# Kernel optimization log

Hardware: AMD Instinct MI355X
Metric: run time of the kernel (lower is better)

## Reference

```python
import jax, jax.numpy as jnp
import numpy as np

B, C, H, W = 8, 256, 64, 64
NUM_LABELS = 16  # labels in {-1, 0..15}; -1 means 'no group'


def setup_inputs() -> dict:
    key = jax.random.key(0)
    kx, kl, kw, kb = jax.random.split(key, 4)
    x = jax.random.normal(kx, (B, C, H, W), dtype=jnp.float32)
    # labels in [-1, NUM_LABELS)
    labels = jax.random.randint(kl, (B * C,), 0, NUM_LABELS + 1) - 1
    # groups=C, kernel 1x1: conv weight is (3C,1,1,1) -> per-output-channel scale; bias (3C,)
    w = jax.random.normal(kw, (3 * C,), dtype=jnp.float32) * 0.5
    b = jax.random.normal(kb, (3 * C,), dtype=jnp.float32) * 0.02
    return {"x": x, "labels": labels, "w": w, "b": b}


def reference(x, labels, w, b):
    # x: (B,C,h,w); labels: (B*C,); w,b: (3C,)
    Bv, Cv, hv, wv = x.shape
    hw = hv * wv
    xf = x.reshape(Bv, Cv, hw)
    # grouped 1x1 conv: out channel o (of 3C) reads input channel o//3
    x_rep = jnp.repeat(xf, 3, axis=1)                      # (B,3C,hw)
    qkv = x_rep * w[None, :, None] + b[None, :, None]      # (B,3C,hw)
    flat = qkv.reshape(Bv * 3 * Cv, hw)                    # matches torch reshape(1,3BC,hw)
    BC = Bv * Cv
    q, k, v = flat[:BC], flat[BC:2 * BC], flat[2 * BC:]    # each (BC, hw)
    valid = labels != -1                                   # (BC,)
    same = (labels[:, None] == labels[None, :]) & valid[:, None] & valid[None, :]
    # per-label-group attention == masked dense attention (softmax over same-label cols only)
    scores = q @ k.T                                       # (BC, BC), no sqrt(d) scaling (as in source)
    neg = jnp.finfo(scores.dtype).min
    scores = jnp.where(same, scores, neg)
    weights = jax.nn.softmax(scores, axis=-1)
    out = weights @ v                                      # (BC, hw)
    out = jnp.where(valid[:, None], out, jnp.zeros((), out.dtype))  # -1 rows stay zero
    return out[None]                                       # (1, BC, hw)
```

## Files before the change

### kernel.cpp

```cpp
#include <hip/hip_runtime.h>
#include <cfloat>

#define B_   8
#define C_   256
#define HW_  4096
#define BC_  2048
#define TC_  768
#define NG_  16
#define MAXG 320
#define UK0  682
#define NUQ  683
#define NUK  684
#define NXU  1366
#define NXALL 2048

#define SPLITK 8
#define NT     11
#define NTILES (NT * NT)
#define KSL    (HW_ / SPLITK)
#define WKC    (KSL / 4)
#define NP1    (NUQ * NUK)

#define MCAP  192
#define CST   192
#define BKP   216

typedef __attribute__((ext_vector_type(8))) short short8;
typedef __attribute__((ext_vector_type(4))) float floatx4;

__device__ __forceinline__ unsigned short f32_to_bf16_rne(float f) {
  unsigned u = __float_as_uint(f);
  unsigned r = (u + 0x7FFFu + ((u >> 16) & 1u)) >> 16;
  return (unsigned short)r;
}

__global__ __launch_bounds__(256) void prep_kernel(
    const float* __restrict__ x, const int* __restrict__ labels,
    unsigned short* __restrict__ xhi, unsigned short* __restrict__ xlo,
    float* __restrict__ sums, int* __restrict__ grp_n,
    int* __restrict__ members, int* __restrict__ posArr, int nhi)
{
  const int t = threadIdx.x;
  if (blockIdx.x < NG_) {
    __shared__ int lab[BC_];
    __shared__ int cnts[256];
    const int g = blockIdx.x;
    for (int idx = t; idx < BC_; idx += 256) lab[idx] = labels[idx];
    __syncthreads();
    const int base = t * 8;
    int cnt = 0;
#pragma unroll
    for (int k = 0; k < 8; k++) cnt += (lab[base + k] == g) ? 1 : 0;
    cnts[t] = cnt;
    for (int off = 1; off < 256; off <<= 1) {
      __syncthreads();
      const int v = (t >= off) ? cnts[t - off] : 0;
      __syncthreads();
      cnts[t] += v;
    }
    __syncthreads();
    int pos = cnts[t] - cnt;
    if (t == 255) grp_n[g] = cnts[255] < MAXG ? cnts[255] : MAXG;
#pragma unroll
    for (int k = 0; k < 8; k++) {
      const int i = base + k;
      if (lab[i] == g) {
        if (pos < MAXG) { members[g * MAXG + pos] = i; posArr[i] = pos; }
        pos++;
      }
    }
    return;
  }

  const int u = blockIdx.x - NG_;
  const float* row = x + (size_t)u * HW_;
  unsigned short* hrow = xhi + (size_t)u * HW_;
  if (u < NXU) {
    unsigned short* lrow = xlo + (size_t)u * HW_;
    float s = 0.f;
#pragma unroll
    for (int i = 0; i < 4; i++) {
      const int col = i * 1024 + t * 4;
      const float4 v = *(const float4*)(row + col);
      s += v.x + v.y + v.z + v.w;
      ushort4 h, l;
      h.x = f32_to_bf16_rne(v.x);
      h.y = f32_to_bf16_rne(v.y);
      h.z = f32_to_bf16_rne(v.z);
      h.w = f32_to_bf16_rne(v.w);
      l.x = f32_to_bf16_rne(v.x - __uint_as_float((unsigned)h.x << 16));
      l.y = f32_to_bf16_rne(v.y - __uint_as_float((unsigned)h.y << 16));
      l.z = f32_to_bf16_rne(v.z - __uint_as_float((unsigned)h.z << 16));
      l.w = f32_to_bf16_rne(v.w - __uint_as_float((unsigned)h.w << 16));
      *(ushort4*)(hrow + col) = h;
      *(ushort4*)(lrow + col) = l;
    }
#pragma unroll
    for (int o = 32; o > 0; o >>= 1) s += __shfl_down(s, o);
    __shared__ float red[4];
    if ((t & 63) == 0) red[t >> 6] = s;
    __syncthreads();
    if (t == 0) sums[u] = red[0] + red[1] + red[2] + red[3];
  } else {
#pragma unroll
    for (int i = 0; i < 4; i++) {
      const int col = i * 1024 + t * 4;
      const float4 v = *(const float4*)(row + col);
      ushort4 h;
      h.x = f32_to_bf16_rne(v.x);
      h.y = f32_to_bf16_rne(v.y);
      h.z = f32_to_bf16_rne(v.z);
      h.w = f32_to_bf16_rne(v.w);
      *(ushort4*)(hrow + col) = h;
    }
  }
}

__global__ __launch_bounds__(256) void gram_mfma_kernel(
    const unsigned short* __restrict__ xhi, const unsigned short* __restrict__ xlo,
    float* __restrict__ P,
    const float* __restrict__ w, const float* __restrict__ bbias,
    const float* __restrict__ sums, const int* __restrict__ grp_n,
    const int* __restrict__ members, float4* __restrict__ gtA,
    float2* __restrict__ gtB)
{
  const int bid  = blockIdx.x;
  const int z    = bid & 7;
  const int tile = bid >> 3;
  const int m0 = (tile % NT) * 64;
  const int n0 = (tile / NT) * 64;

  const int t = threadIdx.x;
  const int wave = t >> 6;
  const int lane = t & 63;
  const int fr = lane & 15;
  const int fq = lane >> 4;

  if (z == 0 && tile < NG_) {
    const int g = tile;
    const int n = grp_n[g];
    for (int p = t; p < n; p += 256) {
      const int j = members[g * MAXG + p];
      const int rk = j + BC_;
      const int jk = rk % TC_;
      const int uk = (rk / TC_) * C_ + jk / 3;
      const int jv = (j + 2 * BC_) % TC_;
      gtA[g * MAXG + p] = make_float4(w[jk], bbias[jk], sums[uk], w[jv]);
      gtB[g * MAXG + p] = make_float2(bbias[jv], __int_as_float(uk - UK0));
    }
  }

  const int kbase = z * KSL + wave * WKC + fq * 8;
  const unsigned short *pah[4], *pal[4], *pbh[4], *pbl[4];
#pragma unroll
  for (int i = 0; i < 4; i++) {
    const int ar = min(m0 + fr + i * 16, NUQ - 1);
    const int br = min(UK0 + n0 + fr + i * 16, NXU - 1);
    pah[i] = xhi + (size_t)ar * HW_ + kbase;
    pal[i] = xlo + (size_t)ar * HW_ + kbase;
    pbh[i] = xhi + (size_t)br * HW_ + kbase;
    pbl[i] = xlo + (size_t)br * HW_ + kbase;
  }

  floatx4 acc[4][4];
#pragma unroll
  for (int i = 0; i < 4; i++)
#pragma unroll
    for (int j = 0; j < 4; j++) acc[i][j] = (floatx4)(0.f);

  for (int kk = 0; kk < WKC; kk += 32) {
    short8 ah[4], al[4], bh[4], bl[4];
#pragma unroll
    for (int i = 0; i < 4; i++) {
      ah[i] = *(const short8*)(pah[i] + kk);
      al[i] = *(const short8*)(pal[i] + kk);
      bh[i] = *(const short8*)(pbh[i] + kk);
      bl[i] = *(const short8*)(pbl[i] + kk);
    }
#pragma unroll
    for (int mt = 0; mt < 4; mt++)
#pragma unroll
      for (int nt = 0; nt < 4; nt++) {
        acc[mt][nt] = __builtin_amdgcn_mfma_f32_16x16x32_bf16(ah[mt], bh[nt], acc[mt][nt], 0, 0, 0);
        acc[mt][nt] = __builtin_amdgcn_mfma_f32_16x16x32_bf16(al[mt], bh[nt], acc[mt][nt], 0, 0, 0);
        acc[mt][nt] = __builtin_amdgcn_mfma_f32_16x16x32_bf16(ah[mt], bl[nt], acc[mt][nt], 0, 0, 0);
      }
  }

  __shared__ float R[2][64][68];
  float* R0 = &R[0][0][0];
  float* R1 = &R[1][0][0];
  if (wave == 0 || wave == 2) {
    float* Rw = (wave == 0) ? R0 : R1;
#pragma unroll
    for (int mt = 0; mt < 4; mt++)
#pragma unroll
      for (int nt = 0; nt < 4; nt++)
#pragma unroll
        for (int r = 0; r < 4; r++)
          Rw[(mt * 16 + fq * 4 + r) * 68 + nt * 16 + fr] = acc[mt][nt][r];
  }
  __syncthreads();
  if (wave == 1 || wave == 3) {
    float* Rw = (wave == 1) ? R0 : R1;
#pragma unroll
    for (int mt = 0; mt < 4; mt++)
#pragma unroll
      for (int nt = 0; nt < 4; nt++)
#pragma unroll
        for (int r = 0; r < 4; r++)
          Rw[(mt * 16 + fq * 4 + r) * 68 + nt * 16 + fr] += acc[mt][nt][r];
  }
  __syncthreads();
  const int em = t >> 2;
  const int en = (t & 3) * 16;
  const int gm = m0 + em;
  if (gm < NUQ) {
    float* dst = P + (size_t)z * NP1 + (size_t)gm * NUK + n0;
#pragma unroll
    for (int i4 = 0; i4 < 4; i4++) {
      const int n = en + i4 * 4;
      if (n0 + n < NUK) {
        float4 v;
        v.x = R0[em * 68 + n + 0] + R1[em * 68 + n + 0];
        v.y = R0[em * 68 + n + 1] + R1[em * 68 + n + 1];
        v.z = R0[em * 68 + n + 2] + R1[em * 68 + n + 2];
        v.w = R0[em * 68 + n + 3] + R1[em * 68 + n + 3];
        *(float4*)(dst + n) = v;
      }
    }
  }
}

__global__ __launch_bounds__(256) void gram_reduce_kernel(
    const float* __restrict__ P, float* __restrict__ S)
{
  const int idx = (blockIdx.x * 256 + threadIdx.x) * 4;
  if (idx < NP1) {
    float4 s = *(const float4*)(P + idx);
#pragma unroll
    for (int sl = 1; sl < SPLITK; sl++) {
      const float4 a = *(const float4*)(P + (size_t)sl * NP1 + idx);
      s.x += a.x; s.y += a.y; s.z += a.z; s.w += a.w;
    }
    *(float4*)(S + idx) = s;
  }
}

__device__ __forceinline__ float blockReduceMax(float v, float* red) {
#pragma unroll
  for (int o = 32; o > 0; o >>= 1) v = fmaxf(v, __shfl_down(v, o));
  if ((threadIdx.x & 63) == 0) red[threadIdx.x >> 6] = v;
  __syncthreads();
  v = fmaxf(fmaxf(red[0], red[1]), fmaxf(red[2], red[3]));
  __syncthreads();
  return v;
}
__device__ __forceinline__ float blockReduceSum(float v, float* red) {
#pragma unroll
  for (int o = 32; o > 0; o >>= 1) v += __shfl_down(v, o);
  if ((threadIdx.x & 63) == 0) red[threadIdx.x >> 6] = v;
  __syncthreads();
  v = red[0] + red[1] + red[2] + red[3];
  __syncthreads();
  return v;
}

__global__ __launch_bounds__(256) void softmax_kernel(
    const int* __restrict__ labels, const float* __restrict__ w,
    const float* __restrict__ bbias, const float* __restrict__ sums,
    const float* __restrict__ S, const int* __restrict__ grp_n,
    const int* __restrict__ posArr, const float4* __restrict__ gtA,
    const float2* __restrict__ gtB, unsigned short* __restrict__ coefh,
    float* __restrict__ cb, float* __restrict__ out)
{
  const int i = blockIdx.x;
  const int t = threadIdx.x;
  const int g = labels[i];
  if (g < 0) {
    const float4 z = make_float4(0.f, 0.f, 0.f, 0.f);
    float4* orow = (float4*)(out + (size_t)i * HW_);
    for (int cidx = t; cidx < HW_ / 4; cidx += 256) orow[cidx] = z;
    return;
  }
  __shared__ float red[4];
  const int n   = grp_n[g];
  const int jq  = i % TC_;
  const int uqi = (i / TC_) * C_ + jq / 3;
  const float wq = w[jq], bq = bbias[jq];
  const float sq = sums[uqi];
  const float* Srow = S + (size_t)uqi * NUK;

  const int jj0 = t, jj1 = t + 256;
  float4 A0, A1; float2 B0, B1;
  float s0 = -FLT_MAX, s1 = -FLT_MAX;
  if (jj0 < n) {
    A0 = gtA[g * MAXG + jj0];
    B0 = gtB[g * MAXG + jj0];
    s0 = wq * A0.x * Srow[__float_as_int(B0.y)] + (wq * A0.y) * sq +
         (bq * A0.x) * A0.z + (bq * A0.y) * 4096.f;
  }
  if (jj1 < n) {
    A1 = gtA[g * MAXG + jj1];
    B1 = gtB[g * MAXG + jj1];
    s1 = wq * A1.x * Srow[__float_as_int(B1.y)] + (wq * A1.y) * sq +
         (bq * A1.x) * A1.z + (bq * A1.y) * 4096.f;
  }
  const float mx = blockReduceMax(fmaxf(s0, s1), red);
  const float e0 = (jj0 < n) ? expf(s0 - mx) : 0.f;
  const float e1 = (jj1 < n) ? expf(s1 - mx) : 0.f;
  const float tot = blockReduceSum(e0 + e1, red);
  const float inv = 1.f / tot;

  const int pos = posArr[i];
  unsigned short* crow = coefh + ((size_t)g * MCAP + pos) * CST;
  float lcb = 0.f;
  if (jj0 < n) {
    const float wgt = e0 * inv;
    if (pos < MCAP && jj0 < CST) crow[jj0] = f32_to_bf16_rne(wgt * A0.w);
    lcb += wgt * B0.x;
  } else if (pos < MCAP && jj0 < CST) {
    crow[jj0] = 0;
  }
  if (jj1 < n) {
    const float wgt = e1 * inv;
    lcb += wgt * B1.x;
  }
  const float cbi = blockReduceSum(lcb, red);
  if (t == 0) cb[i] = cbi;
}

__global__ __launch_bounds__(256) void out_mfma_kernel(
    const float* __restrict__ x, const unsigned short* __restrict__ xh,
    const unsigned short* __restrict__ coefh,
    const float* __restrict__ cb, const int* __restrict__ grp_n,
    const int* __restrict__ members, float* __restrict__ out)
{
  const int g  = blockIdx.x;
  const int c0 = blockIdx.y * 64;
  const int n  = min(grp_n[g], MCAP);
  if (n == 0) return;
  const int Kceil = (n + 31) & ~31;
  const int nk8 = Kceil >> 3;
  const int t = threadIdx.x;
  const int wave = t >> 6;
  const int lane = t & 63;
  const int fr = lane & 15;
  const int fq = lane >> 4;

  __shared__ unsigned short Bt[64][BKP];
  __shared__ int   mem[MCAP];
  __shared__ float cbs[MCAP];

  if (t < n) {
    const int j = members[g * MAXG + t];
    mem[t] = j;
    cbs[t] = cb[j];
  }
  __syncthreads();

  {
    const int colq = t & 15;
    const int kcb  = t >> 4;
    for (int kc = kcb; kc < nk8; kc += 16) {
      if (xh) {
        ushort4 hv[8];
#pragma unroll
        for (int j = 0; j < 8; j++) {
          const int k = kc * 8 + j;
          if (k < n) {
            const int jm = mem[k];
            const int rv = jm + 2 * BC_;
            const int uv = (rv / TC_) * C_ + (rv % TC_) / 3;
            hv[j] = *(const ushort4*)(xh + (size_t)uv * HW_ + c0 + colq * 4);
          } else {
            hv[j] = make_ushort4(0, 0, 0, 0);
          }
        }
#pragma unroll
        for (int c = 0; c < 4; c++) {
          short8 pk;
          pk[0] = (short)(c == 0 ? hv[0].x : c == 1 ? hv[0].y : c == 2 ? hv[0].z : hv[0].w);
          pk[1] = (short)(c == 0 ? hv[1].x : c == 1 ? hv[1].y : c == 2 ? hv[1].z : hv[1].w);
          pk[2] = (short)(c == 0 ? hv[2].x : c == 1 ? hv[2].y : c == 2 ? hv[2].z : hv[2].w);
          pk[3] = (short)(c == 0 ? hv[3].x : c == 1 ? hv[3].y : c == 2 ? hv[3].z : hv[3].w);
          pk[4] = (short)(c == 0 ? hv[4].x : c == 1 ? hv[4].y : c == 2 ? hv[4].z : hv[4].w);
          pk[5] = (short)(c == 0 ? hv[5].x : c == 1 ? hv[5].y : c == 2 ? hv[5].z : hv[5].w);
          pk[6] = (short)(c == 0 ? hv[6].x : c == 1 ? hv[6].y : c == 2 ? hv[6].z : hv[6].w);
          pk[7] = (short)(c == 0 ? hv[7].x : c == 1 ? hv[7].y : c == 2 ? hv[7].z : hv[7].w);
          *(short8*)&Bt[colq * 4 + c][kc * 8] = pk;
        }
      } else {
        float4 vals[8];
#pragma unroll
        for (int j = 0; j < 8; j++) {
          const int k = kc * 8 + j;
          if (k < n) {
            const int jm = mem[k];
            const int rv = jm + 2 * BC_;
            const int uv = (rv / TC_) * C_ + (rv % TC_) / 3;
            vals[j] = *(const float4*)(x + (size_t)uv * HW_ + c0 + colq * 4);
          } else {
            vals[j] = make_float4(0.f, 0.f, 0.f, 0.f);
          }
        }
#pragma unroll
        for (int c = 0; c < 4; c++) {
          short8 pk;
          pk[0] = (short)f32_to_bf16_rne(c == 0 ? vals[0].x : c == 1 ? vals[0].y : c == 2 ? vals[0].z : vals[0].w);
          pk[1] = (short)f32_to_bf16_rne(c == 0 ? vals[1].x : c == 1 ? vals[1].y : c == 2 ? vals[1].z : vals[1].w);
          pk[2] = (short)f32_to_bf16_rne(c == 0 ? vals[2].x : c == 1 ? vals[2].y : c == 2 ? vals[2].z : vals[2].w);
          pk[3] = (short)f32_to_bf16_rne(c == 0 ? vals[3].x : c == 1 ? vals[3].y : c == 2 ? vals[3].z : vals[3].w);
          pk[4] = (short)f32_to_bf16_rne(c == 0 ? vals[4].x : c == 1 ? vals[4].y : c == 2 ? vals[4].z : vals[4].w);
          pk[5] = (short)f32_to_bf16_rne(c == 0 ? vals[5].x : c == 1 ? vals[5].y : c == 2 ? vals[5].z : vals[5].w);
          pk[6] = (short)f32_to_bf16_rne(c == 0 ? vals[6].x : c == 1 ? vals[6].y : c == 2 ? vals[6].z : vals[6].w);
          pk[7] = (short)f32_to_bf16_rne(c == 0 ? vals[7].x : c == 1 ? vals[7].y : c == 2 ? vals[7].z : vals[7].w);
          *(short8*)&Bt[colq * 4 + c][kc * 8] = pk;
        }
      }
    }
  }
  __syncthreads();

  const int colw = wave * 16 + fr;

  for (int m0 = 0; m0 < n; m0 += 32) {
    floatx4 acc0 = (floatx4)(0.f), acc1 = (floatx4)(0.f);
    const unsigned short* pa0 = coefh + ((size_t)g * MCAP + m0 + fr) * CST + fq * 8;
    const unsigned short* pa1 = pa0 + 16 * CST;
    for (int k = 0; k < Kceil; k += 32) {
      const short8 a0 = *(const short8*)(pa0 + k);
      const short8 a1 = *(const short8*)(pa1 + k);
      const short8 b  = *(const short8*)&Bt[colw][fq * 8 + k];
      acc0 = __builtin_amdgcn_mfma_f32_16x16x32_bf16(a0, b, acc0, 0, 0, 0);
      acc1 = __builtin_amdgcn_mfma_f32_16x16x32_bf16(a1, b, acc1, 0, 0, 0);
    }
#pragma unroll
    for (int r = 0; r < 4; r++) {
      int m = m0 + fq * 4 + r;
      if (m < n) out[(size_t)mem[m] * HW_ + c0 + colw] = acc0[r] + cbs[m];
      m += 16;
      if (m < n) out[(size_t)mem[m] * HW_ + c0 + colw] = acc1[r] + cbs[m];
    }
  }
}

extern "C" void kernel_launch(void* const* d_in, const int* in_sizes, int n_in,
                              void* d_out, int out_size, void* d_ws, size_t ws_size,
                              hipStream_t stream)
{
  const float* x      = (const float*)d_in[0];
  const int*   labels = (const int*)d_in[1];
  const float* w      = (const float*)d_in[2];
  const float* bb     = (const float*)d_in[3];
  float* out = (float*)d_out;

  char* wsb = (char*)d_ws;
  size_t off = 0;
  auto carve = [&](size_t bytes) -> void* {
    off = (off + 255) & ~(size_t)255;
    void* p = wsb + off;
    off += bytes;
    return p;
  };
  float* sums    = (float*)carve(NXU * sizeof(float));
  float* S       = (float*)carve((size_t)NP1 * sizeof(float));
  float* P       = (float*)carve((size_t)SPLITK * NP1 * sizeof(float));
  int*   grp_n   = (int*)carve(NG_ * sizeof(int));
  int*   members = (int*)carve((size_t)NG_ * MAXG * sizeof(int));
  int*   posArr  = (int*)carve(BC_ * sizeof(int));
  unsigned short* coefh = (unsigned short*)carve((size_t)NG_ * MCAP * CST * sizeof(unsigned short));
  float* cb      = (float*)carve(BC_ * sizeof(float));
  float4* gtA    = (float4*)carve((size_t)NG_ * MAXG * sizeof(float4));
  float2* gtB    = (float2*)carve((size_t)NG_ * MAXG * sizeof(float2));

  const int big = ws_size >= (size_t)47 * 1024 * 1024;
  const int nhi = big ? NXALL : NXU;
  unsigned short* xhi = (unsigned short*)carve((size_t)nhi * HW_ * sizeof(unsigned short));
  unsigned short* xlo = (unsigned short*)carve((size_t)NXU * HW_ * sizeof(unsigned short));

  prep_kernel<<<NG_ + nhi, 256, 0, stream>>>(x, labels, xhi, xlo, sums,
                                             grp_n, members, posArr, nhi);
  gram_mfma_kernel<<<NTILES * SPLITK, 256, 0, stream>>>(
      xhi, xlo, P, w, bb, sums, grp_n, members, gtA, gtB);
  gram_reduce_kernel<<<(NP1 / 4 + 255) / 256, 256, 0, stream>>>(P, S);
  softmax_kernel<<<BC_, 256, 0, stream>>>(labels, w, bb, sums, S, grp_n,
                                          posArr, gtA, gtB, coefh, cb, out);
  out_mfma_kernel<<<dim3(NG_, HW_ / 64), 256, 0, stream>>>(
      x, big ? xhi : (const unsigned short*)nullptr, coefh, cb, grp_n,
      members, out);
}
```

Before: 161.8 us.

## Replace split-bf16 Gram MFMA with per-row int8 hi/lo quantized i8 MFMA

Each input row is quantized to a 16-bit integer using a per-row max-abs scale, then split into high and low int8 bytes. The Gram product becomes three i32 16x16x64 int8 MFMAs in place of three bf16 16x16x32 MFMAs, which halves operand bytes and doubles K per instruction. The per-row scales are applied in the split-K reduce. The prep kernel now stages rows in shared memory and writes bf16 only for rows the output kernel needs, which changes precision behaviour and adds shared-memory pressure in prep.

```diff
diff --git a/kernel.cpp b/kernel.cpp
--- a/kernel.cpp
+++ b/kernel.cpp
@@ -13,6 +13,7 @@
 #define NUK  684
 #define NXU  1366
 #define NXALL 2048
+#define VLO  1280
 
 #define SPLITK 8
 #define NT     11
@@ -20,6 +21,7 @@
 #define KSL    (HW_ / SPLITK)
 #define WKC    (KSL / 4)
 #define NP1    (NUQ * NUK)
+#define QMAX   32639
 
 #define MCAP  192
 #define CST   192
@@ -27,6 +29,7 @@
 
 typedef __attribute__((ext_vector_type(8))) short short8;
 typedef __attribute__((ext_vector_type(4))) float floatx4;
+typedef __attribute__((ext_vector_type(4))) int   intx4;
 
 __device__ __forceinline__ unsigned short f32_to_bf16_rne(float f) {
   unsigned u = __float_as_uint(f);
@@ -36,9 +39,11 @@
 
 __global__ __launch_bounds__(256) void prep_kernel(
     const float* __restrict__ x, const int* __restrict__ labels,
-    unsigned short* __restrict__ xhi, unsigned short* __restrict__ xlo,
-    float* __restrict__ sums, int* __restrict__ grp_n,
-    int* __restrict__ members, int* __restrict__ posArr, int nhi)
+    char* __restrict__ q8h, char* __restrict__ q8l,
+    unsigned short* __restrict__ xhi, float* __restrict__ sums,
+    float* __restrict__ scA, float* __restrict__ scB,
+    int* __restrict__ grp_n, int* __restrict__ members,
+    int* __restrict__ posArr, int nhi)
 {
   const int t = threadIdx.x;
   if (blockIdx.x < NG_) {
@@ -73,35 +78,73 @@
   }
 
   const int u = blockIdx.x - NG_;
+  if (u >= nhi) return;
   const float* row = x + (size_t)u * HW_;
-  unsigned short* hrow = xhi + (size_t)u * HW_;
+
   if (u < NXU) {
-    unsigned short* lrow = xlo + (size_t)u * HW_;
-    float s = 0.f;
+    __shared__ float xs[HW_];
+    __shared__ float red[4];
+    float s = 0.f, mx = 0.f;
 #pragma unroll
     for (int i = 0; i < 4; i++) {
       const int col = i * 1024 + t * 4;
       const float4 v = *(const float4*)(row + col);
+      *(float4*)(xs + col) = v;
       s += v.x + v.y + v.z + v.w;
-      ushort4 h, l;
-      h.x = f32_to_bf16_rne(v.x);
-      h.y = f32_to_bf16_rne(v.y);
-      h.z = f32_to_bf16_rne(v.z);
-      h.w = f32_to_bf16_rne(v.w);
-      l.x = f32_to_bf16_rne(v.x - __uint_as_float((unsigned)h.x << 16));
-      l.y = f32_to_bf16_rne(v.y - __uint_as_float((unsigned)h.y << 16));
-      l.z = f32_to_bf16_rne(v.z - __uint_as_float((unsigned)h.z << 16));
-      l.w = f32_to_bf16_rne(v.w - __uint_as_float((unsigned)h.w << 16));
-      *(ushort4*)(hrow + col) = h;
-      *(ushort4*)(lrow + col) = l;
+      mx = fmaxf(mx, fmaxf(fmaxf(fabsf(v.x), fabsf(v.y)),
+                           fmaxf(fabsf(v.z), fabsf(v.w))));
     }
 #pragma unroll
     for (int o = 32; o > 0; o >>= 1) s += __shfl_down(s, o);
-    __shared__ float red[4];
     if ((t & 63) == 0) red[t >> 6] = s;
     __syncthreads();
-    if (t == 0) sums[u] = red[0] + red[1] + red[2] + red[3];
+    const float rowsum = red[0] + red[1] + red[2] + red[3];
+    __syncthreads();
+#pragma unroll
+    for (int o = 32; o > 0; o >>= 1) mx = fmaxf(mx, __shfl_down(mx, o));
+    if ((t & 63) == 0) red[t >> 6] = mx;
+    __syncthreads();
+    const float bmax = fmaxf(fmaxf(fmaxf(red[0], red[1]),
+                                   fmaxf(red[2], red[3])), 1e-20f);
+    if (t == 0) {
+      sums[u] = rowsum;
+      const float sc = bmax / (float)QMAX;
+      if (u < NUQ)  scA[u] = sc;
+      if (u >= UK0) scB[u - UK0] = sc;
+    }
+    const float sinv = (float)QMAX / bmax;
+    char* hrow = q8h + (size_t)u * HW_;
+    char* lrow = q8l + (size_t)u * HW_;
+#pragma unroll
+    for (int i = 0; i < 4; i++) {
+      const int col = i * 1024 + t * 4;
+      char4 hc, lc;
+#pragma unroll
+      for (int j = 0; j < 4; j++) {
+        int q = __float2int_rn(xs[col + j] * sinv);
+        q = q > QMAX ? QMAX : (q < -QMAX ? -QMAX : q);
+        const int h = (q + 128) >> 8;
+        ((char*)&hc)[j] = (char)h;
+        ((char*)&lc)[j] = (char)(q - (h << 8));
+      }
+      *(char4*)(hrow + col) = hc;
+      *(char4*)(lrow + col) = lc;
+    }
+    if (xhi && u >= VLO) {
+      unsigned short* hb = xhi + (size_t)u * HW_;
+#pragma unroll
+      for (int i = 0; i < 4; i++) {
+        const int col = i * 1024 + t * 4;
+        ushort4 h;
+        h.x = f32_to_bf16_rne(xs[col + 0]);
+        h.y = f32_to_bf16_rne(xs[col + 1]);
+        h.z = f32_to_bf16_rne(xs[col + 2]);
+        h.w = f32_to_bf16_rne(xs[col + 3]);
+        *(ushort4*)(hb + col) = h;
+      }
+    }
   } else {
+    unsigned short* hb = xhi + (size_t)u * HW_;
 #pragma unroll
     for (int i = 0; i < 4; i++) {
       const int col = i * 1024 + t * 4;
@@ -111,13 +154,13 @@
       h.y = f32_to_bf16_rne(v.y);
       h.z = f32_to_bf16_rne(v.z);
       h.w = f32_to_bf16_rne(v.w);
-      *(ushort4*)(hrow + col) = h;
+      *(ushort4*)(hb + col) = h;
     }
   }
 }
 
 __global__ __launch_bounds__(256) void gram_mfma_kernel(
-    const unsigned short* __restrict__ xhi, const unsigned short* __restrict__ xlo,
+    const char* __restrict__ q8h, const char* __restrict__ q8l,
     float* __restrict__ P,
     const float* __restrict__ w, const float* __restrict__ bbias,
     const float* __restrict__ sums, const int* __restrict__ grp_n,
@@ -150,40 +193,40 @@
     }
   }
 
-  const int kbase = z * KSL + wave * WKC + fq * 8;
-  const unsigned short *pah[4], *pal[4], *pbh[4], *pbl[4];
+  const int kbase = z * KSL + wave * WKC + fq * 16;
+  const char *pah[4], *pal[4], *pbh[4], *pbl[4];
 #pragma unroll
   for (int i = 0; i < 4; i++) {
     const int ar = min(m0 + fr + i * 16, NUQ - 1);
     const int br = min(UK0 + n0 + fr + i * 16, NXU - 1);
-    pah[i] = xhi + (size_t)ar * HW_ + kbase;
-    pal[i] = xlo + (size_t)ar * HW_ + kbase;
-    pbh[i] = xhi + (size_t)br * HW_ + kbase;
-    pbl[i] = xlo + (size_t)br * HW_ + kbase;
-  }
-
-  floatx4 acc[4][4];
+    pah[i] = q8h + (size_t)ar * HW_ + kbase;
+    pal[i] = q8l + (size_t)ar * HW_ + kbase;
+    pbh[i] = q8h + (size_t)br * HW_ + kbase;
+    pbl[i] = q8l + (size_t)br * HW_ + kbase;
+  }
+
+  intx4 acch[4][4], accx[4][4];
 #pragma unroll
   for (int i = 0; i < 4; i++)
 #pragma unroll
-    for (int j = 0; j < 4; j++) acc[i][j] = (floatx4)(0.f);
-
-  for (int kk = 0; kk < WKC; kk += 32) {
-    short8 ah[4], al[4], bh[4], bl[4];
+    for (int j = 0; j < 4; j++) { acch[i][j] = (intx4)(0); accx[i][j] = (intx4)(0); }
+
+  for (int kk = 0; kk < WKC; kk += 64) {
+    intx4 ah[4], al[4], bh[4], bl[4];
 #pragma unroll
     for (int i = 0; i < 4; i++) {
-      ah[i] = *(const short8*)(pah[i] + kk);
-      al[i] = *(const short8*)(pal[i] + kk);
-      bh[i] = *(const short8*)(pbh[i] + kk);
-      bl[i] = *(const short8*)(pbl[i] + kk);
+      ah[i] = *(const intx4*)(pah[i] + kk);
+      al[i] = *(const intx4*)(pal[i] + kk);
+      bh[i] = *(const intx4*)(pbh[i] + kk);
+      bl[i] = *(const intx4*)(pbl[i] + kk);
     }
 #pragma unroll
     for (int mt = 0; mt < 4; mt++)
 #pragma unroll
       for (int nt = 0; nt < 4; nt++) {
-        acc[mt][nt] = __builtin_amdgcn_mfma_f32_16x16x32_bf16(ah[mt], bh[nt], acc[mt][nt], 0, 0, 0);
-        acc[mt][nt] = __builtin_amdgcn_mfma_f32_16x16x32_bf16(al[mt], bh[nt], acc[mt][nt], 0, 0, 0);
-        acc[mt][nt] = __builtin_amdgcn_mfma_f32_16x16x32_bf16(ah[mt], bl[nt], acc[mt][nt], 0, 0, 0);
+        acch[mt][nt] = __builtin_amdgcn_mfma_i32_16x16x64_i8(ah[mt], bh[nt], acch[mt][nt], 0, 0, 0);
+        accx[mt][nt] = __builtin_amdgcn_mfma_i32_16x16x64_i8(ah[mt], bl[nt], accx[mt][nt], 0, 0, 0);
+        accx[mt][nt] = __builtin_amdgcn_mfma_i32_16x16x64_i8(al[mt], bh[nt], accx[mt][nt], 0, 0, 0);
       }
   }
 
@@ -198,7 +241,8 @@
       for (int nt = 0; nt < 4; nt++)
 #pragma unroll
         for (int r = 0; r < 4; r++)
-          Rw[(mt * 16 + fq * 4 + r) * 68 + nt * 16 + fr] = acc[mt][nt][r];
+          Rw[(mt * 16 + fq * 4 + r) * 68 + nt * 16 + fr] =
+              65536.f * (float)acch[mt][nt][r] + 256.f * (float)accx[mt][nt][r];
   }
   __syncthreads();
   if (wave == 1 || wave == 3) {
@@ -209,7 +253,8 @@
       for (int nt = 0; nt < 4; nt++)
 #pragma unroll
         for (int r = 0; r < 4; r++)
-          Rw[(mt * 16 + fq * 4 + r) * 68 + nt * 16 + fr] += acc[mt][nt][r];
+          Rw[(mt * 16 + fq * 4 + r) * 68 + nt * 16 + fr] +=
+              65536.f * (float)acch[mt][nt][r] + 256.f * (float)accx[mt][nt][r];
   }
   __syncthreads();
   const int em = t >> 2;
@@ -233,7 +278,8 @@
 }
 
 __global__ __launch_bounds__(256) void gram_reduce_kernel(
-    const float* __restrict__ P, float* __restrict__ S)
+    const float* __restrict__ P, float* __restrict__ S,
+    const float* __restrict__ scA, const float* __restrict__ scB)
 {
   const int idx = (blockIdx.x * 256 + threadIdx.x) * 4;
   if (idx < NP1) {
@@ -243,6 +289,11 @@
       const float4 a = *(const float4*)(P + (size_t)sl * NP1 + idx);
       s.x += a.x; s.y += a.y; s.z += a.z; s.w += a.w;
     }
+    const int m = idx / NUK;
+    const int n = idx - m * NUK;
+    const float sa = scA[m];
+    const float4 sb = *(const float4*)(scB + n);
+    s.x *= sa * sb.x; s.y *= sa * sb.y; s.z *= sa * sb.z; s.w *= sa * sb.w;
     *(float4*)(S + idx) = s;
   }
 }
@@ -464,6 +515,8 @@
     return p;
   };
   float* sums    = (float*)carve(NXU * sizeof(float));
+  float* scA     = (float*)carve(NUQ * sizeof(float));
+  float* scB     = (float*)carve(NUK * sizeof(float));
   float* S       = (float*)carve((size_t)NP1 * sizeof(float));
   float* P       = (float*)carve((size_t)SPLITK * NP1 * sizeof(float));
   int*   grp_n   = (int*)carve(NG_ * sizeof(int));
@@ -473,20 +526,22 @@
   float* cb      = (float*)carve(BC_ * sizeof(float));
   float4* gtA    = (float4*)carve((size_t)NG_ * MAXG * sizeof(float4));
   float2* gtB    = (float2*)carve((size_t)NG_ * MAXG * sizeof(float2));
+  char*  q8h     = (char*)carve((size_t)NXU * HW_);
+  char*  q8l     = (char*)carve((size_t)NXU * HW_);
 
   const int big = ws_size >= (size_t)47 * 1024 * 1024;
+  unsigned short* xhi = big
+      ? (unsigned short*)carve((size_t)NXALL * HW_ * sizeof(unsigned short))
+      : (unsigned short*)nullptr;
   const int nhi = big ? NXALL : NXU;
-  unsigned short* xhi = (unsigned short*)carve((size_t)nhi * HW_ * sizeof(unsigned short));
-  unsigned short* xlo = (unsigned short*)carve((size_t)NXU * HW_ * sizeof(unsigned short));
-
-  prep_kernel<<<NG_ + nhi, 256, 0, stream>>>(x, labels, xhi, xlo, sums,
-                                             grp_n, members, posArr, nhi);
+
+  prep_kernel<<<NG_ + nhi, 256, 0, stream>>>(x, labels, q8h, q8l, xhi, sums,
+                                             scA, scB, grp_n, members, posArr, nhi);
   gram_mfma_kernel<<<NTILES * SPLITK, 256, 0, stream>>>(
-      xhi, xlo, P, w, bb, sums, grp_n, members, gtA, gtB);
-  gram_reduce_kernel<<<(NP1 / 4 + 255) / 256, 256, 0, stream>>>(P, S);
+      q8h, q8l, P, w, bb, sums, grp_n, members, gtA, gtB);
+  gram_reduce_kernel<<<(NP1 / 4 + 255) / 256, 256, 0, stream>>>(P, S, scA, scB);
   softmax_kernel<<<BC_, 256, 0, stream>>>(labels, w, bb, sums, S, grp_n,
                                           posArr, gtA, gtB, coefh, cb, out);
   out_mfma_kernel<<<dim3(NG_, HW_ / 64), 256, 0, stream>>>(
-      x, big ? xhi : (const unsigned short*)nullptr, coefh, cb, grp_n,
-      members, out);
-}
+      x, xhi, coefh, cb, grp_n, members, out);
+}
```

New measurement: 155.5 us. 3.9% less time.
